# Kernel optimization log

Measured on AMD Instinct MI355X. Metric: run time of the kernel, lower is better.

Reference implementation:

```python
import jax, jax.numpy as jnp
import numpy as np

N_HEADS, N_MODES, C_IN, C_OUT, SPD = 4, 32, 32, 32, 3


def setup_inputs() -> dict:
    key = jax.random.key(0)
    ks = jax.random.split(key, 9)
    B, NX, NY, NZ = 2, 48, 48, 48
    omega, c = 30.0 / 300.0, 6.0
    a = jax.random.normal(ks[0], (B, NX, NY, NZ, C_IN), jnp.float32)
    x = jax.random.uniform(ks[1], (B, NX, NY, NZ, SPD), jnp.float32)
    y = jax.random.uniform(ks[2], (B, NX, NY, NZ, SPD), jnp.float32)
    a_scale = np.sqrt(c / (C_IN + N_MODES)).astype(np.float32)
    x_scale = (np.sqrt(c / (SPD + N_MODES)) * omega).astype(np.float32)
    u_scale = np.sqrt(c / (N_HEADS * N_MODES + C_OUT)).astype(np.float32)
    a_modes = a_scale * (2 * jax.random.uniform(ks[3], (N_HEADS, N_MODES, C_IN), jnp.float32) - 1)
    x_modes = x_scale * (2 * jax.random.uniform(ks[4], (N_HEADS, N_MODES, SPD), jnp.float32) - 1)
    y_modes = x_scale * (2 * jax.random.uniform(ks[5], (N_HEADS, N_MODES, SPD), jnp.float32) - 1)
    u_modes = u_scale * (2 * jax.random.uniform(ks[6], (N_HEADS, N_MODES, C_OUT), jnp.float32) - 1)
    lim = 1.0 / np.sqrt(C_IN)
    fc_w = jax.random.uniform(ks[7], (C_OUT, C_IN), jnp.float32, -lim, lim)
    fc_b = jax.random.uniform(ks[8], (C_OUT,), jnp.float32, -lim, lim)
    return dict(a=a, x=x, y=y, a_modes=a_modes, x_modes=x_modes,
                y_modes=y_modes, u_modes=u_modes, fc_w=fc_w, fc_b=fc_b)


def _spectral_attention(a, x, y, a_modes, x_modes, y_modes, u_modes):
    # a: (b,nx,ny,nz,i); x,y: (b,nx,ny,nz,d)
    A = jnp.einsum('bxyzi,hfi->bhxyzf', a, a_modes)  # real
    X = jnp.exp(-2j * np.pi * jnp.einsum('bxyzd,hgd->bhxyzg', x, x_modes))
    Y = jnp.exp(2j * np.pi * jnp.einsum('bxyzd,hgd->bhxyzg', y, y_modes))
    n_xyz = y.shape[1] * y.shape[2] * y.shape[3]
    AX = jnp.einsum('bhxyzf,bhxyzg->bhfg', A.astype(X.dtype), X)
    U = jnp.einsum('bhfg,bhxyzg->bhxyzf', AX, Y).real / n_xyz
    return jnp.einsum('bhxyzf,hfo->bxyzo', U, u_modes)


def reference(a, x, y, a_modes, x_modes, y_modes, u_modes, fc_w, fc_b):
    att = _spectral_attention(a, x, y, a_modes, x_modes, y_modes, u_modes)
    skip = jnp.einsum('bxyzi,oi->bxyzo', a, fc_w) + fc_b
    return jax.nn.gelu(att + skip, approximate=False)
```

## Files before the change

### kernel.cpp

```cpp
#include <hip/hip_runtime.h>
#include <hip/hip_bf16.h>
#include <math.h>

#define NHEADS 4
#define NM 32
#define CIN 32
#define COUT 32
#define BATCH 2
#define NPTS (48*48*48)
#define PAD 36
#define SEGS_AX (NPTS/256)
#define SEGS_OUT (NPTS/128)
#define INV_N (1.0f / (float)NPTS)

typedef unsigned short ushort_t;
typedef __attribute__((ext_vector_type(8))) short short8;
typedef __attribute__((ext_vector_type(16))) float floatx16;

#define MFMA32 __builtin_amdgcn_mfma_f32_32x32x16_bf16

union frag8 { short8 v; uint2 u2[2]; unsigned u[4]; ushort_t s[8]; };

__device__ __forceinline__ floatx16 zero16() {
    floatx16 z;
#pragma unroll
    for (int i = 0; i < 16; ++i) z[i] = 0.0f;
    return z;
}
__device__ __forceinline__ ushort_t f2bf(float f) {
    __hip_bfloat16 h = __float2bfloat16(f);
    return *(ushort_t*)&h;
}
__device__ __forceinline__ float bf2f(ushort_t u) {
    union { unsigned i; float f; } v; v.i = ((unsigned)u) << 16; return v.f;
}
__device__ __forceinline__ unsigned pk2(float a, float b) {
    return (unsigned)f2bf(a) | ((unsigned)f2bf(b) << 16);
}
__device__ __forceinline__ short8 frag_from_f32(const float* __restrict__ p, float scale) {
    float4 f0 = ((const float4*)p)[0], f1 = ((const float4*)p)[1];
    frag8 r;
    r.u[0] = pk2(f0.x * scale, f0.y * scale);
    r.u[1] = pk2(f0.z * scale, f0.w * scale);
    r.u[2] = pk2(f1.x * scale, f1.y * scale);
    r.u[3] = pk2(f1.z * scale, f1.w * scale);
    return r.v;
}
__device__ __forceinline__ short8 frag_lds(const ushort_t* p) {
    frag8 r;
    r.u2[0] = *(const uint2*)p;
    r.u2[1] = *(const uint2*)(p + 4);
    return r.v;
}

__global__ __launch_bounds__(256, 4) void k_ax(
    const float* __restrict__ a, const float* __restrict__ x,
    const float* __restrict__ a_modes, const float* __restrict__ x_modes,
    float* __restrict__ AX, float* __restrict__ part, int use_part)
{
    __shared__ ushort_t s_a[256][PAD];
    __shared__ float4   s_x4[256];
    __shared__ ushort_t s_At[NHEADS][NM][PAD];

    const int t = threadIdx.x;
    const int w = t >> 6;
    const int l = t & 63;
    const int l31 = l & 31, lh = l >> 5;
    const int b  = blockIdx.x / SEGS_AX;
    const int sb = blockIdx.x % SEGS_AX;
    const int pbase = b * NPTS + sb * 256;

    {
        const float* arow = a + (size_t)(pbase + t) * CIN;
        unsigned* dst = (unsigned*)&s_a[t][0];
#pragma unroll
        for (int v = 0; v < 8; ++v) {
            float4 f = ((const float4*)arow)[v];
            dst[2*v]   = pk2(f.x, f.y);
            dst[2*v+1] = pk2(f.z, f.w);
        }
        for (int idx = t; idx < 256*3; idx += 256) {
            const float v = x[(size_t)pbase * 3 + idx];
            const int pt = idx / 3;
            ((float*)&s_x4[pt])[idx - 3*pt] = v;
        }
    }
    short8 amf[2];
#pragma unroll
    for (int kh = 0; kh < 2; ++kh)
        amf[kh] = frag_from_f32(a_modes + (w*NM + l31)*CIN + kh*16 + lh*8, 1.0f);
    const float xm0 = x_modes[(w*NM + l31)*3 + 0];
    const float xm1 = x_modes[(w*NM + l31)*3 + 1];
    const float xm2 = x_modes[(w*NM + l31)*3 + 2];

    floatx16 accre = zero16(), accim = zero16();
    __syncthreads();

    for (int c = 0; c < 8; ++c) {
        const int p0 = c * 32;
        short8 xre[2], xim[2];
#pragma unroll
        for (int kh = 0; kh < 2; ++kh) {
            frag8 re_, im_;
#pragma unroll
            for (int j = 0; j < 8; j += 2) {
                const int pl = p0 + kh*16 + lh*8 + j;
                const float4 v0 = s_x4[pl], v1 = s_x4[pl + 1];
                const float q0 = v0.x*xm0 + v0.y*xm1 + v0.z*xm2;
                const float q1 = v1.x*xm0 + v1.y*xm1 + v1.z*xm2;
                re_.u[j>>1] = pk2( __builtin_amdgcn_cosf(q0),  __builtin_amdgcn_cosf(q1));
                im_.u[j>>1] = pk2(-__builtin_amdgcn_sinf(q0), -__builtin_amdgcn_sinf(q1));
            }
            xre[kh] = re_.v; xim[kh] = im_.v;
        }
        floatx16 dA = zero16();
#pragma unroll
        for (int kh = 0; kh < 2; ++kh) {
            short8 af = frag_lds(&s_a[p0 + l31][kh*16 + lh*8]);
            dA = MFMA32(amf[kh], af, dA, 0, 0, 0);
        }
#pragma unroll
        for (int r = 0; r < 16; ++r) {
            const int fr = (r & 3) + 8*(r >> 2) + 4*lh;
            s_At[w][fr][l31] = f2bf(dA[r]);
        }
#pragma unroll
        for (int kh = 0; kh < 2; ++kh) {
            short8 atf = frag_lds(&s_At[w][l31][kh*16 + lh*8]);
            accre = MFMA32(atf, xre[kh], accre, 0, 0, 0);
            accim = MFMA32(atf, xim[kh], accim, 0, 0, 0);
        }
    }

    if (use_part) {
        float* pr = part + (size_t)blockIdx.x * 8192;
#pragma unroll
        for (int r = 0; r < 16; ++r) {
            const int fr = (r & 3) + 8*(r >> 2) + 4*lh;
            const int idx = (w*NM + fr)*NM + l31;
            pr[idx]        = accre[r];
            pr[idx + 4096] = accim[r];
        }
    } else {
        float* AXre = AX;
        float* AXim = AX + BATCH*NHEADS*NM*NM;
#pragma unroll
        for (int r = 0; r < 16; ++r) {
            const int fr = (r & 3) + 8*(r >> 2) + 4*lh;
            const int idx = b*4096 + (w*NM + fr)*NM + l31;
            atomicAdd(&AXre[idx], accre[r]);
            atomicAdd(&AXim[idx], accim[r]);
        }
    }
}

__global__ void k_red(const float* __restrict__ part, float* __restrict__ AX)
{
    __shared__ float s_red[8][32];
    const int t = threadIdx.x, q = t >> 5, l = t & 31;
    const int o = blockIdx.x * 32 + l;
    const int bb = o >> 13, idx = o & 8191;
    float acc = 0.f;
#pragma unroll 6
    for (int sb = q; sb < SEGS_AX; sb += 8)
        acc += part[((size_t)(bb*SEGS_AX + sb))*8192 + idx];
    s_red[q][l] = acc;
    __syncthreads();
    if (t < 32) {
        float s = 0.f;
#pragma unroll
        for (int qq = 0; qq < 8; ++qq) s += s_red[qq][t];
        const int oo = blockIdx.x * 32 + t;
        const int b2 = oo >> 13, i2 = oo & 8191;
        if (i2 < 4096) AX[b2*4096 + i2] = s;
        else           AX[8192 + b2*4096 + (i2 - 4096)] = s;
    }
}

__global__ void k_w(const float* __restrict__ AX, const float* __restrict__ u_modes,
                    ushort_t* __restrict__ W)
{
    const int t = threadIdx.x, w = t >> 6, l = t & 63;
    const int l31 = l & 31, lh = l >> 5;
    const int pair = blockIdx.x * 4 + w;
    const int b = pair >> 2, h = pair & 3;
    const float* AXre = AX + b*4096 + h*1024;
    const float* AXim = AX + BATCH*4096 + b*4096 + h*1024;
    const float* um   = u_modes + h*1024;

    short8 umf[2], axr[2], axi[2];
#pragma unroll
    for (int kh = 0; kh < 2; ++kh) {
        frag8 u_, r_, i_;
#pragma unroll
        for (int j = 0; j < 8; j += 2) {
            const int f0 = kh*16 + lh*8 + j, f1 = f0 + 1;
            u_.u[j>>1] = pk2(um[f0*32 + l31], um[f1*32 + l31]);
            r_.u[j>>1] = pk2(AXre[f0*32 + l31]*INV_N, AXre[f1*32 + l31]*INV_N);
            i_.u[j>>1] = pk2(AXim[f0*32 + l31]*INV_N, AXim[f1*32 + l31]*INV_N);
        }
        umf[kh] = u_.v; axr[kh] = r_.v; axi[kh] = i_.v;
    }
    floatx16 wre = zero16(), wim = zero16();
#pragma unroll
    for (int kh = 0; kh < 2; ++kh) {
        wre = MFMA32(umf[kh], axr[kh], wre, 0, 0, 0);
        wim = MFMA32(umf[kh], axi[kh], wim, 0, 0, 0);
    }
    ushort_t* Wre = W + (size_t)pair * 1024;
    ushort_t* Wim = Wre + 8192;
#pragma unroll
    for (int r = 0; r < 16; ++r) {
        const int o = (r & 3) + 8*(r >> 2) + 4*lh;
        Wre[o*32 + l31] = f2bf(wre[r]);
        Wim[o*32 + l31] = f2bf(wim[r]);
    }
}

__global__ __launch_bounds__(256, 4) void k_out(
    const float* __restrict__ a, const float* __restrict__ y,
    const float* __restrict__ y_modes, const ushort_t* __restrict__ Wg,
    const float* __restrict__ fc_w, const float* __restrict__ fc_b,
    float* __restrict__ out)
{
    __shared__ ushort_t s_Wre[NHEADS][NM][PAD];
    __shared__ ushort_t s_Wim[NHEADS][NM][PAD];
    __shared__ float4   s_ym4[NHEADS][NM];
    __shared__ float4   s_y4[128];
    __shared__ ushort_t s_ah[128][PAD];

    const int t = threadIdx.x, w = t >> 6, l = t & 63;
    const int l31 = l & 31, lh = l >> 5;
    const int b  = blockIdx.x / SEGS_OUT;
    const int sb = blockIdx.x % SEGS_OUT;
    const int pblock = b * NPTS + sb * 128;
    const int pwave  = pblock + w * 32;

    {
        const unsigned* wr = (const unsigned*)Wg + b*2048;
        const unsigned* wi = (const unsigned*)(Wg + 8192) + b*2048;
        for (int idx2 = t; idx2 < 2048; idx2 += 256) {
            const int h = idx2 >> 9, o = (idx2 >> 4) & 31, g2 = (idx2 & 15) * 2;
            *(unsigned*)&s_Wre[h][o][g2] = wr[idx2];
            *(unsigned*)&s_Wim[h][o][g2] = wi[idx2];
        }
    }
    if (t < 128) {
        const int h = t >> 5, g = t & 31;
        const float* p = y_modes + (h*NM + g)*3;
        float4 v; v.x = p[0]; v.y = p[1]; v.z = p[2]; v.w = 0.f;
        s_ym4[h][g] = v;
    }
    for (int idx = t; idx < 128*3; idx += 256) {
        const float v = y[(size_t)pblock * 3 + idx];
        const int pt = idx / 3;
        ((float*)&s_y4[pt])[idx - 3*pt] = v;
    }
    if (t < 128) {
        const float* arow = a + (size_t)(pblock + t) * CIN;
        unsigned* dst = (unsigned*)&s_ah[t][0];
#pragma unroll
        for (int v = 0; v < 8; ++v) {
            float4 f = ((const float4*)arow)[v];
            dst[2*v]   = pk2(f.x, f.y);
            dst[2*v+1] = pk2(f.z, f.w);
        }
    }
    short8 whi[2], wlo[2];
#pragma unroll
    for (int kh = 0; kh < 2; ++kh) {
        const float* p = fc_w + l31*CIN + kh*16 + lh*8;
        float4 f0 = ((const float4*)p)[0], f1 = ((const float4*)p)[1];
        float v[8] = {f0.x,f0.y,f0.z,f0.w,f1.x,f1.y,f1.z,f1.w};
        frag8 hi, lo;
#pragma unroll
        for (int j = 0; j < 8; ++j) {
            const ushort_t hb = f2bf(v[j]);
            hi.s[j] = hb;
            lo.s[j] = f2bf(v[j] - bf2f(hb));
        }
        whi[kh] = hi.v; wlo[kh] = lo.v;
    }
    const float fb = fc_b[l31];

    __syncthreads();
    const float4 y3 = s_y4[w*32 + l31];

    floatx16 acc = zero16();
#pragma unroll
    for (int kh = 0; kh < 2; ++kh) {
        short8 af = frag_lds(&s_ah[w*32 + l31][kh*16 + lh*8]);
        acc = MFMA32(af, whi[kh], acc, 0, 0, 0);
        acc = MFMA32(af, wlo[kh], acc, 0, 0, 0);
    }
    for (int h = 0; h < NHEADS; ++h) {
        short8 yre[2], yim[2];
#pragma unroll
        for (int kh = 0; kh < 2; ++kh) {
            frag8 re_, im_;
#pragma unroll
            for (int j = 0; j < 8; j += 2) {
                const int g0 = kh*16 + lh*8 + j;
                const float4 m0 = s_ym4[h][g0], m1 = s_ym4[h][g0 + 1];
                const float p0 = y3.x*m0.x + y3.y*m0.y + y3.z*m0.z;
                const float p1 = y3.x*m1.x + y3.y*m1.y + y3.z*m1.z;
                re_.u[j>>1] = pk2( __builtin_amdgcn_cosf(p0),  __builtin_amdgcn_cosf(p1));
                im_.u[j>>1] = pk2(-__builtin_amdgcn_sinf(p0), -__builtin_amdgcn_sinf(p1));
            }
            yre[kh] = re_.v; yim[kh] = im_.v;
        }
#pragma unroll
        for (int kh = 0; kh < 2; ++kh) {
            short8 wrf = frag_lds(&s_Wre[h][l31][kh*16 + lh*8]);
            short8 wif = frag_lds(&s_Wim[h][l31][kh*16 + lh*8]);
            acc = MFMA32(yre[kh], wrf, acc, 0, 0, 0);
            acc = MFMA32(yim[kh], wif, acc, 0, 0, 0);
        }
    }
#pragma unroll
    for (int r = 0; r < 16; ++r) {
        const int ptr_ = (r & 3) + 8*(r >> 2) + 4*lh;
        const float z = acc[r] + fb;
        out[(size_t)(pwave + ptr_) * COUT + l31] =
            0.5f * z * (1.0f + erff(z * 0.70710678118654752f));
    }
}

extern "C" void kernel_launch(void* const* d_in, const int* in_sizes, int n_in,
                              void* d_out, int out_size, void* d_ws, size_t ws_size,
                              hipStream_t stream) {
    (void)in_sizes; (void)n_in; (void)out_size;
    const float* a       = (const float*)d_in[0];
    const float* x       = (const float*)d_in[1];
    const float* y       = (const float*)d_in[2];
    const float* a_modes = (const float*)d_in[3];
    const float* x_modes = (const float*)d_in[4];
    const float* y_modes = (const float*)d_in[5];
    const float* u_modes = (const float*)d_in[6];
    const float* fc_w    = (const float*)d_in[7];
    const float* fc_b    = (const float*)d_in[8];
    float* out  = (float*)d_out;
    float*    AX   = (float*)d_ws;
    ushort_t* W    = (ushort_t*)((char*)d_ws + 65536);
    float*    part = (float*)((char*)d_ws + 98304);

    const size_t need = 98304 + (size_t)BATCH * SEGS_AX * 8192 * sizeof(float);
    const int use_part = (ws_size >= need) ? 1 : 0;

    hipMemsetAsync(AX, 0, 65536, stream);
    k_ax<<<BATCH * SEGS_AX, 256, 0, stream>>>(a, x, a_modes, x_modes, AX, part, use_part);
    if (use_part) k_red<<<512, 256, 0, stream>>>(part, AX);
    k_w<<<2, 256, 0, stream>>>(AX, u_modes, W);
    k_out<<<BATCH * SEGS_OUT, 256, 0, stream>>>(a, y, y_modes, W, fc_w, fc_b, out);
}
```

Measured before the change: 154.3 us.

## Reassociate a_modes projection out of point loop into small W kernel

The a_modes projection is moved out of the per-point loop. k_ax now accumulates raw a^T·exp(-i x·modes) (32 input channels by 32 modes per head) directly from a transposed LDS copy of a. The a_modes multiply is applied once on the reduced 32x32 matrices inside a rewritten k_w that uses 8 blocks and FP32 FMAs. This removes the per-chunk MFMA, the bf16 round-trip through LDS and a barrier-free LDS exchange from the hot loop. Segments grow to 288 points, and the memset is skipped when partials are used. The transposed LDS store is strided 2-byte writes, which may cause bank conflicts in the load phase.

```diff
diff --git a/kernel.cpp b/kernel.cpp
--- a/kernel.cpp
+++ b/kernel.cpp
@@ -9,7 +9,9 @@
 #define BATCH 2
 #define NPTS (48*48*48)
 #define PAD 36
-#define SEGS_AX (NPTS/256)
+#define PTS_AX 288
+#define SEGS_AX (NPTS/PTS_AX)
+#define PADT 292
 #define SEGS_OUT (NPTS/128)
 #define INV_N (1.0f / (float)NPTS)
 
@@ -36,15 +38,6 @@
 }
 __device__ __forceinline__ unsigned pk2(float a, float b) {
     return (unsigned)f2bf(a) | ((unsigned)f2bf(b) << 16);
-}
-__device__ __forceinline__ short8 frag_from_f32(const float* __restrict__ p, float scale) {
-    float4 f0 = ((const float4*)p)[0], f1 = ((const float4*)p)[1];
-    frag8 r;
-    r.u[0] = pk2(f0.x * scale, f0.y * scale);
-    r.u[1] = pk2(f0.z * scale, f0.w * scale);
-    r.u[2] = pk2(f1.x * scale, f1.y * scale);
-    r.u[3] = pk2(f1.z * scale, f1.w * scale);
-    return r.v;
 }
 __device__ __forceinline__ short8 frag_lds(const ushort_t* p) {
     frag8 r;
@@ -55,12 +48,11 @@
 
 __global__ __launch_bounds__(256, 4) void k_ax(
     const float* __restrict__ a, const float* __restrict__ x,
-    const float* __restrict__ a_modes, const float* __restrict__ x_modes,
+    const float* __restrict__ x_modes,
     float* __restrict__ AX, float* __restrict__ part, int use_part)
 {
-    __shared__ ushort_t s_a[256][PAD];
-    __shared__ float4   s_x4[256];
-    __shared__ ushort_t s_At[NHEADS][NM][PAD];
+    __shared__ ushort_t s_aT[CIN][PADT];
+    __shared__ float4   s_x4[PTS_AX];
 
     const int t = threadIdx.x;
     const int w = t >> 6;
@@ -68,27 +60,24 @@
     const int l31 = l & 31, lh = l >> 5;
     const int b  = blockIdx.x / SEGS_AX;
     const int sb = blockIdx.x % SEGS_AX;
-    const int pbase = b * NPTS + sb * 256;
-
-    {
-        const float* arow = a + (size_t)(pbase + t) * CIN;
-        unsigned* dst = (unsigned*)&s_a[t][0];
+    const int pbase = b * NPTS + sb * PTS_AX;
+
+    for (int pt = t; pt < PTS_AX; pt += 256) {
+        const float* arow = a + (size_t)(pbase + pt) * CIN;
 #pragma unroll
         for (int v = 0; v < 8; ++v) {
             float4 f = ((const float4*)arow)[v];
-            dst[2*v]   = pk2(f.x, f.y);
-            dst[2*v+1] = pk2(f.z, f.w);
-        }
-        for (int idx = t; idx < 256*3; idx += 256) {
-            const float v = x[(size_t)pbase * 3 + idx];
-            const int pt = idx / 3;
-            ((float*)&s_x4[pt])[idx - 3*pt] = v;
-        }
-    }
-    short8 amf[2];
-#pragma unroll
-    for (int kh = 0; kh < 2; ++kh)
-        amf[kh] = frag_from_f32(a_modes + (w*NM + l31)*CIN + kh*16 + lh*8, 1.0f);
+            s_aT[4*v+0][pt] = f2bf(f.x);
+            s_aT[4*v+1][pt] = f2bf(f.y);
+            s_aT[4*v+2][pt] = f2bf(f.z);
+            s_aT[4*v+3][pt] = f2bf(f.w);
+        }
+    }
+    for (int idx = t; idx < PTS_AX*3; idx += 256) {
+        const float v = x[(size_t)pbase * 3 + idx];
+        const int pt = idx / 3;
+        ((float*)&s_x4[pt])[idx - 3*pt] = v;
+    }
     const float xm0 = x_modes[(w*NM + l31)*3 + 0];
     const float xm1 = x_modes[(w*NM + l31)*3 + 1];
     const float xm2 = x_modes[(w*NM + l31)*3 + 2];
@@ -96,7 +85,7 @@
     floatx16 accre = zero16(), accim = zero16();
     __syncthreads();
 
-    for (int c = 0; c < 8; ++c) {
+    for (int c = 0; c < PTS_AX/32; ++c) {
         const int p0 = c * 32;
         short8 xre[2], xim[2];
 #pragma unroll
@@ -113,20 +102,9 @@
             }
             xre[kh] = re_.v; xim[kh] = im_.v;
         }
-        floatx16 dA = zero16();
 #pragma unroll
         for (int kh = 0; kh < 2; ++kh) {
-            short8 af = frag_lds(&s_a[p0 + l31][kh*16 + lh*8]);
-            dA = MFMA32(amf[kh], af, dA, 0, 0, 0);
-        }
-#pragma unroll
-        for (int r = 0; r < 16; ++r) {
-            const int fr = (r & 3) + 8*(r >> 2) + 4*lh;
-            s_At[w][fr][l31] = f2bf(dA[r]);
-        }
-#pragma unroll
-        for (int kh = 0; kh < 2; ++kh) {
-            short8 atf = frag_lds(&s_At[w][l31][kh*16 + lh*8]);
+            short8 atf = frag_lds(&s_aT[l31][p0 + kh*16 + lh*8]);
             accre = MFMA32(atf, xre[kh], accre, 0, 0, 0);
             accim = MFMA32(atf, xim[kh], accim, 0, 0, 0);
         }
@@ -136,20 +114,20 @@
         float* pr = part + (size_t)blockIdx.x * 8192;
 #pragma unroll
         for (int r = 0; r < 16; ++r) {
-            const int fr = (r & 3) + 8*(r >> 2) + 4*lh;
-            const int idx = (w*NM + fr)*NM + l31;
+            const int ir = (r & 3) + 8*(r >> 2) + 4*lh;
+            const int idx = (w*NM + ir)*NM + l31;
             pr[idx]        = accre[r];
             pr[idx + 4096] = accim[r];
         }
     } else {
-        float* AXre = AX;
-        float* AXim = AX + BATCH*NHEADS*NM*NM;
+        float* Mre = AX;
+        float* Mim = AX + BATCH*NHEADS*NM*NM;
 #pragma unroll
         for (int r = 0; r < 16; ++r) {
-            const int fr = (r & 3) + 8*(r >> 2) + 4*lh;
-            const int idx = b*4096 + (w*NM + fr)*NM + l31;
-            atomicAdd(&AXre[idx], accre[r]);
-            atomicAdd(&AXim[idx], accim[r]);
+            const int ir = (r & 3) + 8*(r >> 2) + 4*lh;
+            const int idx = b*4096 + (w*NM + ir)*NM + l31;
+            atomicAdd(&Mre[idx], accre[r]);
+            atomicAdd(&Mim[idx], accim[r]);
         }
     }
 }
@@ -177,43 +155,56 @@
     }
 }
 
-__global__ void k_w(const float* __restrict__ AX, const float* __restrict__ u_modes,
-                    ushort_t* __restrict__ W)
+__global__ void k_w(const float* __restrict__ AX, const float* __restrict__ a_modes,
+                    const float* __restrict__ u_modes, ushort_t* __restrict__ W)
 {
-    const int t = threadIdx.x, w = t >> 6, l = t & 63;
-    const int l31 = l & 31, lh = l >> 5;
-    const int pair = blockIdx.x * 4 + w;
-    const int b = pair >> 2, h = pair & 3;
-    const float* AXre = AX + b*4096 + h*1024;
-    const float* AXim = AX + BATCH*4096 + b*4096 + h*1024;
-    const float* um   = u_modes + h*1024;
-
-    short8 umf[2], axr[2], axi[2];
-#pragma unroll
-    for (int kh = 0; kh < 2; ++kh) {
-        frag8 u_, r_, i_;
-#pragma unroll
-        for (int j = 0; j < 8; j += 2) {
-            const int f0 = kh*16 + lh*8 + j, f1 = f0 + 1;
-            u_.u[j>>1] = pk2(um[f0*32 + l31], um[f1*32 + l31]);
-            r_.u[j>>1] = pk2(AXre[f0*32 + l31]*INV_N, AXre[f1*32 + l31]*INV_N);
-            i_.u[j>>1] = pk2(AXim[f0*32 + l31]*INV_N, AXim[f1*32 + l31]*INV_N);
-        }
-        umf[kh] = u_.v; axr[kh] = r_.v; axi[kh] = i_.v;
-    }
-    floatx16 wre = zero16(), wim = zero16();
-#pragma unroll
-    for (int kh = 0; kh < 2; ++kh) {
-        wre = MFMA32(umf[kh], axr[kh], wre, 0, 0, 0);
-        wim = MFMA32(umf[kh], axi[kh], wim, 0, 0, 0);
-    }
-    ushort_t* Wre = W + (size_t)pair * 1024;
-    ushort_t* Wim = Wre + 8192;
-#pragma unroll
-    for (int r = 0; r < 16; ++r) {
-        const int o = (r & 3) + 8*(r >> 2) + 4*lh;
-        Wre[o*32 + l31] = f2bf(wre[r]);
-        Wim[o*32 + l31] = f2bf(wim[r]);
+    __shared__ float sM[2][NM][NM];
+    __shared__ float sT[2][NM][NM + 1];
+    const int t = threadIdx.x;
+    const int b = blockIdx.x >> 2, h = blockIdx.x & 3;
+    const float* Mre = AX + b*4096 + h*1024;
+    const float* Mim = AX + BATCH*4096 + b*4096 + h*1024;
+    for (int i = t; i < 1024; i += 256) {
+        sM[0][i >> 5][i & 31] = Mre[i];
+        sM[1][i >> 5][i & 31] = Mim[i];
+    }
+    __syncthreads();
+    const int fo = t >> 3;
+    const int g0 = (t & 7) * 4;
+    {
+        const float* am = a_modes + (h*NM + fo)*CIN;
+        float tr[4] = {0,0,0,0}, ti[4] = {0,0,0,0};
+#pragma unroll 8
+        for (int i = 0; i < CIN; ++i) {
+            const float wv = am[i];
+#pragma unroll
+            for (int j = 0; j < 4; ++j) {
+                tr[j] += wv * sM[0][i][g0+j];
+                ti[j] += wv * sM[1][i][g0+j];
+            }
+        }
+#pragma unroll
+        for (int j = 0; j < 4; ++j) { sT[0][fo][g0+j] = tr[j]; sT[1][fo][g0+j] = ti[j]; }
+    }
+    __syncthreads();
+    {
+        float wr[4] = {0,0,0,0}, wi[4] = {0,0,0,0};
+#pragma unroll 8
+        for (int f = 0; f < NM; ++f) {
+            const float wv = u_modes[(h*NM + f)*COUT + fo];
+#pragma unroll
+            for (int j = 0; j < 4; ++j) {
+                wr[j] += wv * sT[0][f][g0+j];
+                wi[j] += wv * sT[1][f][g0+j];
+            }
+        }
+        ushort_t* Wre = W + (size_t)blockIdx.x * 1024;
+        ushort_t* Wim = Wre + 8192;
+#pragma unroll
+        for (int j = 0; j < 4; ++j) {
+            Wre[fo*NM + g0 + j] = f2bf(wr[j] * INV_N);
+            Wim[fo*NM + g0 + j] = f2bf(wi[j] * INV_N);
+        }
     }
 }
 
@@ -347,9 +338,9 @@
     const size_t need = 98304 + (size_t)BATCH * SEGS_AX * 8192 * sizeof(float);
     const int use_part = (ws_size >= need) ? 1 : 0;
 
-    hipMemsetAsync(AX, 0, 65536, stream);
-    k_ax<<<BATCH * SEGS_AX, 256, 0, stream>>>(a, x, a_modes, x_modes, AX, part, use_part);
+    if (!use_part) hipMemsetAsync(AX, 0, 65536, stream);
+    k_ax<<<BATCH * SEGS_AX, 256, 0, stream>>>(a, x, x_modes, AX, part, use_part);
     if (use_part) k_red<<<512, 256, 0, stream>>>(part, AX);
-    k_w<<<2, 256, 0, stream>>>(AX, u_modes, W);
+    k_w<<<8, 256, 0, stream>>>(AX, a_modes, u_modes, W);
     k_out<<<BATCH * SEGS_OUT, 256, 0, stream>>>(a, y, y_modes, W, fc_w, fc_b, out);
 }
```

After: 150.3 us. -2.6%, faster.
